# Kernel optimization log

Measured on AMD Instinct MI355X. Metric: run time of the kernel, lower is better.

## Reference

```python
import jax, jax.numpy as jnp
import numpy as np

B, T, D = 2, 2048, 1024
P, ALPHA, P_R = 512, 4, 64
HID = 16 * D
EPS = 1e-6


def rmsnorm(x, w):
    norm = jnp.sqrt(jnp.mean(x * x, axis=-1, keepdims=True) + EPS)
    return x * w / norm


def ssm_lowrank(t, F, b_r, c_r):
    # gated elementwise recurrence h_t = F_t * h_{t-1} + t_t, then low-rank correction
    Fs = jnp.moveaxis(F, 1, 0)   # (T,B,P)
    ts = jnp.moveaxis(t, 1, 0)   # (T,B,P)

    def step(h, inp):
        f, u = inp
        h = f * h + u
        return h, h

    h0 = jnp.zeros((t.shape[0], t.shape[2]), dtype=t.dtype)
    _, hs = jax.lax.scan(step, h0, (Fs, ts))
    h = jnp.moveaxis(hs, 0, 1)   # (B,T,P)
    t_tilde = t + jnp.einsum('btp,pr,rq->btq', h, b_r, c_r)
    return t_tilde


def setup_inputs() -> dict:
    key = jax.random.key(0)
    ks = jax.random.split(key, 11)
    s = lambda fan: 1.0 / np.sqrt(fan)
    return {
        'x':       jax.random.normal(ks[0], (B, T, D), jnp.float32),
        'w_norm1': jnp.ones((D,), jnp.float32),
        'w_toP':   jax.random.normal(ks[1], (D, P), jnp.float32) * s(D),
        'w_emb':   jax.random.normal(ks[2], (D, ALPHA * P), jnp.float32) * s(D),
        'w_f':     jax.random.normal(ks[3], (D, P), jnp.float32) * s(D),
        'b_r':     jax.random.normal(ks[4], (P, P_R), jnp.float32) * s(P),
        'c_r':     jax.random.normal(ks[5], (P_R, P), jnp.float32) * s(P_R),
        'w_fromP': jax.random.normal(ks[6], (P, D), jnp.float32) * s(P),
        'w_norm2': jnp.ones((D,), jnp.float32),
        'w_fc1':   jax.random.normal(ks[7], (D, HID), jnp.float32) * s(D),
        'w_fc2':   jax.random.normal(ks[8], (HID, D), jnp.float32) * s(HID),
    }


def reference(x, w_norm1, w_toP, w_emb, w_f, b_r, c_r, w_fromP, w_norm2, w_fc1, w_fc2):
    # ---- pre-LN CEPTA context path ----
    h1 = rmsnorm(x, w_norm1)
    pre_path = jnp.einsum('btd,dp->btp', h1, w_toP)                 # to_P
    U = jnp.einsum('btd,dk->btk', h1, w_emb).reshape(B, T, ALPHA, P)  # cepta_dense U
    Fgate = jax.nn.sigmoid(jnp.einsum('btd,dp->btp', h1, w_f))      # cepta_dense F
    Y = jax.nn.gelu(U)                                              # cepta_dense Y
    t = jnp.sum(Y, axis=2) + pre_path                               # router reduce='sum'
    t_tilde = ssm_lowrank(t, Fgate, b_r, c_r)                       # low-rank SSM
    y = jnp.einsum('btp,pd->btd', t_tilde, w_fromP)                 # from_P
    x = x + y
    # ---- pre-LN GELU MLP ----
    h2 = rmsnorm(x, w_norm2)
    z = jnp.einsum('bth,hd->btd', jax.nn.gelu(jnp.einsum('btd,dh->bth', h2, w_fc1)), w_fc2)
    return x + z
```

## Files before the change

### kernel.cpp

```cpp
#include <hip/hip_runtime.h>

typedef unsigned short u16;
typedef __bf16 bf16x8 __attribute__((ext_vector_type(8)));
typedef float f32x4 __attribute__((ext_vector_type(4)));
typedef int i32x4 __attribute__((ext_vector_type(4)));

__device__ inline u16 f2bf(float f) {
  union { float f; unsigned u; } v; v.f = f;
  unsigned u = v.u;
  unsigned r = (u + 0x7FFFu + ((u >> 16) & 1u)) >> 16;
  return (u16)r;
}
__device__ inline float bf2f(u16 u) {
  union { unsigned u; float f; } v; v.u = ((unsigned)u) << 16; return v.f;
}

__device__ inline float gelu_f(float x) {
  float t = 0.7978845608028654f * (x + 0.044715f * x * x * x);
  float a = __expf(-2.f * fabsf(t));
  float th = (1.f - a) / (1.f + a);
  th = copysignf(th, t);
  return 0.5f * x * (1.f + th);
}
__device__ inline float sigmoid_f(float x) { return 1.f / (1.f + __expf(-x)); }

__device__ __forceinline__ void gld16(const u16* g, u16* l) {
  __builtin_amdgcn_global_load_lds((const __attribute__((address_space(1))) void*)g,
                                   (__attribute__((address_space(3))) void*)l, 16, 0, 0);
}
__device__ __forceinline__ bf16x8 ld_frag(const u16* p) {
  return __builtin_bit_cast(bf16x8, *(const i32x4*)p);
}

__global__ void transpose_cvt(const float* __restrict__ in, u16* __restrict__ out,
                              int R, int C, int ldout) {
  __shared__ float tile[32][33];
  int c0 = blockIdx.x * 32, r0 = blockIdx.y * 32;
  int tx = threadIdx.x, ty = threadIdx.y;
#pragma unroll
  for (int i = 0; i < 32; i += 8) {
    int r = r0 + ty + i, c = c0 + tx;
    tile[ty + i][tx] = (r < R && c < C) ? in[(long)r * C + c] : 0.f;
  }
  __syncthreads();
#pragma unroll
  for (int i = 0; i < 32; i += 8) {
    int cc = c0 + ty + i, rr = r0 + tx;
    if (cc < C && rr < R) out[(long)cc * ldout + rr] = f2bf(tile[tx][ty + i]);
  }
}

__global__ __launch_bounds__(256) void rmsnorm_k(const float* __restrict__ x,
                                                 const float* __restrict__ w,
                                                 u16* __restrict__ out) {
  int row = blockIdx.x;
  int tid = threadIdx.x;
  const float4* xv = (const float4*)(x + (long)row * 1024);
  float4 v = xv[tid];
  float ss = v.x * v.x + v.y * v.y + v.z * v.z + v.w * v.w;
#pragma unroll
  for (int off = 32; off > 0; off >>= 1) ss += __shfl_down(ss, off);
  __shared__ float red[4];
  if ((tid & 63) == 0) red[tid >> 6] = ss;
  __syncthreads();
  float tot = red[0] + red[1] + red[2] + red[3];
  float scale = rsqrtf(tot * (1.f / 1024.f) + 1e-6f);
  const float4* wv4 = (const float4*)w;
  float4 wv = wv4[tid];
  ushort4 o;
  o.x = f2bf(v.x * wv.x * scale);
  o.y = f2bf(v.y * wv.y * scale);
  o.z = f2bf(v.z * wv.z * scale);
  o.w = f2bf(v.w * wv.w * scale);
  *((ushort4*)(out + (long)row * 1024) + tid) = o;
}

#define EPI_BF16 0
#define EPI_ROUTE1 1
#define EPI_ADD_BF16 2
#define EPI_ADD_F32 3
#define EPI_GELU_BF16 4
#define EPI_PART 5

#define VM4() asm volatile("s_waitcnt vmcnt(4)" ::: "memory")
#define VM0() asm volatile("s_waitcnt vmcnt(0)" ::: "memory")
#define BAR()                                   \
  asm volatile("" ::: "memory");                \
  __builtin_amdgcn_s_barrier();                 \
  asm volatile("" ::: "memory")

template <int EPI>
__global__ __launch_bounds__(512, 2) void gemm256(
    const u16* __restrict__ A, const u16* __restrict__ Bt,
    u16* __restrict__ obf, float* __restrict__ of32,
    int N, int K, int lda, int ldb) {
  __shared__ __align__(16) u16 sA[2][16384];
  __shared__ __align__(16) u16 sB[2][16384];
  const int tid = threadIdx.x;
  const int lane = tid & 63;
  const int wave = tid >> 6;
  const int wm = wave >> 2, wn = wave & 3;
  const int lane15 = lane & 15;

  const int gx = gridDim.x, gy = gridDim.y, gz = gridDim.z;
  const int nwg = gx * gy * gz;
  int orig = (blockIdx.z * gy + blockIdx.y) * gx + blockIdx.x;
  int id = ((nwg & 7) == 0) ? ((orig & 7) * (nwg >> 3) + (orig >> 3)) : orig;
  const int bx = id % gx;
  const int by = (id / gx) % gy;
  const int bz = id / (gx * gy);
  const int bm0 = by * 256, bn0 = bx * 256;
  const int kper = K / gz, koff = bz * kper;

  f32x4 acc[8][4];
  f32x4 zero = {0.f, 0.f, 0.f, 0.f};
#pragma unroll
  for (int m = 0; m < 8; ++m)
#pragma unroll
    for (int n = 0; n < 4; ++n) acc[m][n] = zero;

  const int grow = tid >> 2;
  const int gck = ((tid & 3) ^ ((tid >> 3) & 3)) << 3;
  const u16* pA0 = A + (long)(bm0 + grow) * lda + koff + gck;
  const u16* pB0 = Bt + (long)(bn0 + grow) * ldb + koff + gck;
  const u16* pA1 = pA0 + (long)128 * lda;
  const u16* pB1 = pB0 + (long)128 * ldb;
  const int wofs = wave << 9;

  const int coff = (((lane >> 4) ^ ((lane15 >> 1) & 3)) << 3);
  const u16* baseA = &sA[0][wm * 8192 + lane15 * 32 + coff];
  const u16* baseB = &sB[0][((wn >> 1) * 2) * 4096 + ((wn & 1) * 64 + lane15) * 32 + coff];

  const int nk = kper >> 6;
  const int nu = nk >> 1;

  gld16(pA0, &sA[0][0 * 4096 + wofs]);
  gld16(pA1, &sA[0][2 * 4096 + wofs]);
  gld16(pB0, &sB[0][0 * 4096 + wofs]);
  gld16(pB1, &sB[0][2 * 4096 + wofs]);
  gld16(pA0 + 32, &sA[0][1 * 4096 + wofs]);
  gld16(pA1 + 32, &sA[0][3 * 4096 + wofs]);
  gld16(pB0 + 32, &sB[0][1 * 4096 + wofs]);
  gld16(pB1 + 32, &sB[0][3 * 4096 + wofs]);

  bf16x8 av[4], bv[4];
#define DSRD_B256(P, kk)                                                     \
  _Pragma("unroll") for (int n = 0; n < 4; ++n)                              \
      bv[n] = ld_frag(baseB + (P)*16384 + (kk)*4096 + n * 512);
#define DSRD_A256(P, kk, mh)                                                 \
  _Pragma("unroll") for (int m = 0; m < 4; ++m)                              \
      av[m] = ld_frag(baseA + (P)*16384 + (kk)*4096 + (mh)*2048 + m * 512);
#define MFMA16(mh)                                                                   \
  __builtin_amdgcn_s_setprio(1);                                                     \
  _Pragma("unroll") for (int m = 0; m < 4; ++m)                                      \
      _Pragma("unroll") for (int n = 0; n < 4; ++n)                                  \
          acc[(mh)*4 + m][n] =                                                       \
              __builtin_amdgcn_mfma_f32_16x16x32_bf16(av[m], bv[n], acc[(mh)*4 + m][n], 0, 0, 0); \
  __builtin_amdgcn_s_setprio(0);

#define TILE256(P, STG, TOFS, LASTVM0)                       \
  VM4(); BAR();                                              \
  DSRD_B256(P, 0); DSRD_A256(P, 0, 0);                       \
  if (STG) { gld16(pA0 + (TOFS), &sA[(P) ^ 1][0 * 4096 + wofs]); gld16(pA1 + (TOFS), &sA[(P) ^ 1][2 * 4096 + wofs]); } \
  MFMA16(0);                                                 \
  DSRD_A256(P, 0, 1);                                        \
  if (STG) { gld16(pB0 + (TOFS), &sB[(P) ^ 1][0 * 4096 + wofs]); gld16(pB1 + (TOFS), &sB[(P) ^ 1][2 * 4096 + wofs]); } \
  MFMA16(1);                                                 \
  if (LASTVM0) { VM0(); } else { VM4(); }                    \
  BAR();                                                     \
  DSRD_B256(P, 1); DSRD_A256(P, 1, 0);                       \
  if (STG) { gld16(pA0 + (TOFS) + 32, &sA[(P) ^ 1][1 * 4096 + wofs]); gld16(pA1 + (TOFS) + 32, &sA[(P) ^ 1][3 * 4096 + wofs]); } \
  MFMA16(0);                                                 \
  DSRD_A256(P, 1, 1);                                        \
  if (STG) { gld16(pB0 + (TOFS) + 32, &sB[(P) ^ 1][1 * 4096 + wofs]); gld16(pB1 + (TOFS) + 32, &sB[(P) ^ 1][3 * 4096 + wofs]); } \
  MFMA16(1);

  for (int u = 0; u < nu; ++u) {
    const bool lp = (u == nu - 1);
    TILE256(0, true, 64, false);
    TILE256(1, !lp, 128, lp);
    pA0 += 128; pA1 += 128; pB0 += 128; pB1 += 128;
  }
#undef DSRD_B256
#undef DSRD_A256
#undef MFMA16
#undef TILE256

#pragma unroll
  for (int M = 0; M < 8; ++M) {
    int row_b = bm0 + wm * 128 + M * 16 + ((lane >> 4) << 2);
#pragma unroll
    for (int n = 0; n < 4; ++n) {
      int col = bn0 + wn * 64 + n * 16 + lane15;
#pragma unroll
      for (int j = 0; j < 4; ++j) {
        int row = row_b + j;
        float v = acc[M][n][j];
        if constexpr (EPI == EPI_GELU_BF16) {
          obf[(long)row * N + col] = f2bf(gelu_f(v));
        } else {
          of32[(long)bz * (4096L * 1024) + (long)row * N + col] = v;
        }
      }
    }
  }
}

template <int EPI>
__global__ __launch_bounds__(256, 2) void gemm128(
    const u16* __restrict__ A, const u16* __restrict__ Bt,
    u16* __restrict__ obf, float* __restrict__ of32, const float* __restrict__ add,
    u16* __restrict__ og, float* __restrict__ ofl,
    int N, int K, int lda, int ldb) {
  __shared__ __align__(16) u16 sA[2][8192];
  __shared__ __align__(16) u16 sB[2][8192];
  const int tid = threadIdx.x;
  const int lane = tid & 63;
  const int wave = tid >> 6;
  const int wm = wave >> 1, wn = wave & 1;
  const int lane15 = lane & 15;

  const int gx = gridDim.x, gy = gridDim.y;
  const int nwg = gx * gy;
  int orig = blockIdx.y * gx + blockIdx.x;
  int id = ((nwg & 7) == 0) ? ((orig & 7) * (nwg >> 3) + (orig >> 3)) : orig;
  const int bx = id % gx;
  const int by = id / gx;
  const int bm0 = by * 128, bn0 = bx * 128;

  f32x4 acc[4][4];
  f32x4 zero = {0.f, 0.f, 0.f, 0.f};
#pragma unroll
  for (int m = 0; m < 4; ++m)
#pragma unroll
    for (int n = 0; n < 4; ++n) acc[m][n] = zero;

  const int grow = tid >> 2;
  const int gck = ((tid & 3) ^ ((tid >> 3) & 3)) << 3;
  const u16* pA0 = A + (long)(bm0 + grow) * lda + gck;
  const u16* pB0 = Bt + (long)(bn0 + grow) * ldb + gck;
  const u16* pA1 = pA0 + (long)64 * lda;
  const u16* pB1 = pB0 + (long)64 * ldb;
  const int wofs = wave << 9;

  const int coff = (((lane >> 4) ^ ((lane15 >> 1) & 3)) << 3);
  const u16* baseA = &sA[0][wm * 2048 + lane15 * 32 + coff];
  const u16* baseB = &sB[0][wn * 2048 + lane15 * 32 + coff];

  const int nk = K >> 6;
  const int nu = nk >> 1;

  gld16(pA0, &sA[0][0 * 4096 + 0 * 2048 + wofs]);
  gld16(pA1, &sA[0][0 * 4096 + 1 * 2048 + wofs]);
  gld16(pB0, &sB[0][0 * 4096 + 0 * 2048 + wofs]);
  gld16(pB1, &sB[0][0 * 4096 + 1 * 2048 + wofs]);
  gld16(pA0 + 32, &sA[0][1 * 4096 + 0 * 2048 + wofs]);
  gld16(pA1 + 32, &sA[0][1 * 4096 + 1 * 2048 + wofs]);
  gld16(pB0 + 32, &sB[0][1 * 4096 + 0 * 2048 + wofs]);
  gld16(pB1 + 32, &sB[0][1 * 4096 + 1 * 2048 + wofs]);

  bf16x8 av[4], bv[4];
#define DSRD128(P, kk)                                                              \
  _Pragma("unroll") for (int m = 0; m < 4; ++m)                                     \
      av[m] = ld_frag(baseA + (P)*8192 + (kk)*4096 + m * 512);                      \
  _Pragma("unroll") for (int n = 0; n < 4; ++n)                                     \
      bv[n] = ld_frag(baseB + (P)*8192 + (kk)*4096 + n * 512);
#define MFMA16x()                                                                   \
  __builtin_amdgcn_s_setprio(1);                                                    \
  _Pragma("unroll") for (int m = 0; m < 4; ++m)                                     \
      _Pragma("unroll") for (int n = 0; n < 4; ++n)                                 \
          acc[m][n] = __builtin_amdgcn_mfma_f32_16x16x32_bf16(av[m], bv[n], acc[m][n], 0, 0, 0); \
  __builtin_amdgcn_s_setprio(0);
#define TILE128(P, STG, TOFS, LASTVM0)                                              \
  VM4(); BAR();                                                                     \
  DSRD128(P, 0);                                                                    \
  if (STG) {                                                                        \
    gld16(pA0 + (TOFS), &sA[(P) ^ 1][0 * 4096 + 0 * 2048 + wofs]);                  \
    gld16(pA1 + (TOFS), &sA[(P) ^ 1][0 * 4096 + 1 * 2048 + wofs]);                  \
    gld16(pB0 + (TOFS), &sB[(P) ^ 1][0 * 4096 + 0 * 2048 + wofs]);                  \
    gld16(pB1 + (TOFS), &sB[(P) ^ 1][0 * 4096 + 1 * 2048 + wofs]);                  \
  }                                                                                 \
  MFMA16x();                                                                        \
  if (LASTVM0) { VM0(); } else { VM4(); }                                           \
  BAR();                                                                            \
  DSRD128(P, 1);                                                                    \
  if (STG) {                                                                        \
    gld16(pA0 + (TOFS) + 32, &sA[(P) ^ 1][1 * 4096 + 0 * 2048 + wofs]);             \
    gld16(pA1 + (TOFS) + 32, &sA[(P) ^ 1][1 * 4096 + 1 * 2048 + wofs]);             \
    gld16(pB0 + (TOFS) + 32, &sB[(P) ^ 1][1 * 4096 + 0 * 2048 + wofs]);             \
    gld16(pB1 + (TOFS) + 32, &sB[(P) ^ 1][1 * 4096 + 1 * 2048 + wofs]);             \
  }                                                                                 \
  MFMA16x();

  for (int u = 0; u < nu; ++u) {
    const bool lp = (u == nu - 1);
    TILE128(0, true, 64, false);
    TILE128(1, !lp, 128, lp);
    pA0 += 128; pA1 += 128; pB0 += 128; pB1 += 128;
  }
#undef DSRD128
#undef MFMA16x
#undef TILE128

#pragma unroll
  for (int M = 0; M < 4; ++M) {
    int row_b = bm0 + wm * 64 + M * 16 + ((lane >> 4) << 2);
#pragma unroll
    for (int n = 0; n < 4; ++n) {
      int col = bn0 + wn * 64 + n * 16 + lane15;
#pragma unroll
      for (int j = 0; j < 4; ++j) {
        int row = row_b + j;
        float v = acc[M][n][j];
        if constexpr (EPI == EPI_BF16) {
          obf[(long)row * N + col] = f2bf(v);
        } else if constexpr (EPI == EPI_ADD_BF16) {
          long idx = (long)row * N + col;
          obf[idx] = f2bf(add[idx] + v);
        } else if constexpr (EPI == EPI_ADD_F32) {
          long idx = (long)row * N + col;
          of32[idx] = add[idx] + v;
        } else if constexpr (EPI == EPI_ROUTE1) {
          if (col < 512) of32[(long)row * 512 + col] = v;
          else if (col < 2560) og[(long)row * 2048 + (col - 512)] = f2bf(gelu_f(v));
          else ofl[(long)row * 512 + (col - 2560)] = sigmoid_f(v);
        }
      }
    }
  }
}

__global__ __launch_bounds__(256) void reduce4_k(const float* __restrict__ base,
                                                 const float* __restrict__ p,
                                                 float* __restrict__ o) {
  long i = (long)blockIdx.x * 256 + threadIdx.x;
  const long PL = 4096L * 1024 / 4;
  float4 b = ((const float4*)base)[i];
  float4 q0 = ((const float4*)p)[i];
  float4 q1 = ((const float4*)p)[i + PL];
  float4 q2 = ((const float4*)p)[i + 2 * PL];
  float4 q3 = ((const float4*)p)[i + 3 * PL];
  float4 r;
  r.x = b.x + q0.x + q1.x + q2.x + q3.x;
  r.y = b.y + q0.y + q1.y + q2.y + q3.y;
  r.z = b.z + q0.z + q1.z + q2.z + q3.z;
  r.w = b.w + q0.w + q1.w + q2.w + q3.w;
  ((float4*)o)[i] = r;
}

__global__ __launch_bounds__(256) void router_k(float* __restrict__ tb, const u16* __restrict__ G) {
  int i = blockIdx.x * 256 + threadIdx.x;
  int r = i >> 7, pq = i & 127;
  float4 t = ((float4*)tb)[i];
#pragma unroll
  for (int a = 0; a < 4; ++a) {
    ushort4 g = *((const ushort4*)(G + (long)r * 2048 + a * 512) + pq);
    t.x += bf2f(g.x); t.y += bf2f(g.y); t.z += bf2f(g.z); t.w += bf2f(g.w);
  }
  ((float4*)tb)[i] = t;
}

__global__ void scan_chunk(const float* __restrict__ tb, const float* __restrict__ F,
                           float* __restrict__ abuf, float* __restrict__ ubuf) {
  int b = blockIdx.x >> 5, c = blockIdx.x & 31, pidx = threadIdx.x;
  const float* fp = F + ((long)(b * 2048 + c * 64) * 512) + pidx;
  const float* up = tb + ((long)(b * 2048 + c * 64) * 512) + pidx;
  float A = 1.f, U = 0.f;
#pragma unroll 8
  for (int s = 0; s < 64; ++s) {
    float f = fp[(long)s * 512], u = up[(long)s * 512];
    A = f * A;
    U = f * U + u;
  }
  abuf[(b * 32 + c) * 512 + pidx] = A;
  ubuf[(b * 32 + c) * 512 + pidx] = U;
}

__global__ void scan_combine(const float* __restrict__ abuf, const float* __restrict__ ubuf,
                             float* __restrict__ hstart) {
  int b = blockIdx.x, pidx = threadIdx.x;
  float h = 0.f;
  for (int c = 0; c < 32; ++c) {
    hstart[(b * 32 + c) * 512 + pidx] = h;
    h = abuf[(b * 32 + c) * 512 + pidx] * h + ubuf[(b * 32 + c) * 512 + pidx];
  }
}

__global__ void scan_apply(const float* __restrict__ tb, const float* __restrict__ F,
                           const float* __restrict__ hstart, u16* __restrict__ hbf) {
  int b = blockIdx.x >> 5, c = blockIdx.x & 31, pidx = threadIdx.x;
  const float* fp = F + ((long)(b * 2048 + c * 64) * 512) + pidx;
  const float* up = tb + ((long)(b * 2048 + c * 64) * 512) + pidx;
  u16* op = hbf + ((long)(b * 2048 + c * 64) * 512) + pidx;
  float h = hstart[(b * 32 + c) * 512 + pidx];
#pragma unroll 8
  for (int s = 0; s < 64; ++s) {
    float f = fp[(long)s * 512], u = up[(long)s * 512];
    h = f * h + u;
    op[(long)s * 512] = f2bf(h);
  }
}

extern "C" void kernel_launch(void* const* d_in, const int* in_sizes, int n_in,
                              void* d_out, int out_size, void* d_ws, size_t ws_size,
                              hipStream_t stream) {
  const float* x       = (const float*)d_in[0];
  const float* w_norm1 = (const float*)d_in[1];
  const float* w_toP   = (const float*)d_in[2];
  const float* w_emb   = (const float*)d_in[3];
  const float* w_f     = (const float*)d_in[4];
  const float* b_r     = (const float*)d_in[5];
  const float* c_r     = (const float*)d_in[6];
  const float* w_fromP = (const float*)d_in[7];
  const float* w_norm2 = (const float*)d_in[8];
  const float* w_fc1   = (const float*)d_in[9];
  const float* w_fc2   = (const float*)d_in[10];
  float* out = (float*)d_out;

  char* base = (char*)d_ws;
  size_t off = 0;
  auto alloc = [&](size_t bytes) {
    void* r = base + off;
    off += (bytes + 255) & ~(size_t)255;
    return r;
  };
  u16* W1T     = (u16*)alloc((size_t)3072 * 1024 * 2);
  u16* WfromPT = (u16*)alloc((size_t)1024 * 512 * 2);
  u16* Wfc1T   = (u16*)alloc((size_t)16384 * 1024 * 2);
  u16* Wfc2T   = (u16*)alloc((size_t)1024 * 16384 * 2);
  u16* BrT     = (u16*)alloc((size_t)128 * 512 * 2);
  u16* CrT     = (u16*)alloc((size_t)512 * 128 * 2);
  u16* h1      = (u16*)alloc((size_t)4096 * 1024 * 2);
  float* G     = (float*)alloc((size_t)4096 * 2048 * 4);
  float* F     = (float*)alloc((size_t)4096 * 512 * 4);
  float* tb    = (float*)alloc((size_t)4096 * 512 * 4);
  float* abuf  = (float*)alloc((size_t)2 * 32 * 512 * 4);
  float* ubuf  = (float*)alloc((size_t)2 * 32 * 512 * 4);
  float* hstart= (float*)alloc((size_t)2 * 32 * 512 * 4);
  u16* hbf     = (u16*)alloc((size_t)4096 * 512 * 2);
  u16* g1buf   = (u16*)alloc((size_t)4096 * 128 * 2);
  u16* tt      = (u16*)alloc((size_t)4096 * 512 * 2);
  float* xmid  = (float*)alloc((size_t)4096 * 1024 * 4);
  u16* h2      = (u16*)alloc((size_t)4096 * 1024 * 2);
  u16* a3      = (u16*)alloc((size_t)4096 * 8192 * 2);
  float* part  = (float*)h1;
  u16* Gbf     = (u16*)G;
  (void)ws_size; (void)in_sizes; (void)n_in; (void)out_size;

  dim3 tpb(32, 8);
  transpose_cvt<<<dim3(16, 32), tpb, 0, stream>>>(w_toP, W1T, 1024, 512, 1024);
  transpose_cvt<<<dim3(64, 32), tpb, 0, stream>>>(w_emb, W1T + (size_t)512 * 1024, 1024, 2048, 1024);
  transpose_cvt<<<dim3(16, 32), tpb, 0, stream>>>(w_f, W1T + (size_t)2560 * 1024, 1024, 512, 1024);
  transpose_cvt<<<dim3(32, 16), tpb, 0, stream>>>(w_fromP, WfromPT, 512, 1024, 512);
  transpose_cvt<<<dim3(512, 32), tpb, 0, stream>>>(w_fc1, Wfc1T, 1024, 16384, 1024);
  transpose_cvt<<<dim3(32, 512), tpb, 0, stream>>>(w_fc2, Wfc2T, 16384, 1024, 16384);
  hipMemsetAsync(BrT, 0, (size_t)128 * 512 * 2, stream);
  hipMemsetAsync(CrT, 0, (size_t)512 * 128 * 2, stream);
  transpose_cvt<<<dim3(2, 16), tpb, 0, stream>>>(b_r, BrT, 512, 64, 512);
  transpose_cvt<<<dim3(16, 2), tpb, 0, stream>>>(c_r, CrT, 64, 512, 128);

  rmsnorm_k<<<4096, 256, 0, stream>>>(x, w_norm1, h1);

  gemm128<EPI_ROUTE1><<<dim3(24, 32), 256, 0, stream>>>(h1, W1T, nullptr, tb, nullptr, Gbf, F,
                                                        3072, 1024, 1024, 1024);
  router_k<<<2048, 256, 0, stream>>>(tb, Gbf);

  scan_chunk<<<64, 512, 0, stream>>>(tb, F, abuf, ubuf);
  scan_combine<<<2, 512, 0, stream>>>(abuf, ubuf, hstart);
  scan_apply<<<64, 512, 0, stream>>>(tb, F, hstart, hbf);

  gemm128<EPI_BF16><<<dim3(1, 32), 256, 0, stream>>>(hbf, BrT, g1buf, nullptr, nullptr, nullptr, nullptr,
                                                     128, 512, 512, 512);
  gemm128<EPI_ADD_BF16><<<dim3(4, 32), 256, 0, stream>>>(g1buf, CrT, tt, nullptr, tb, nullptr, nullptr,
                                                         512, 128, 128, 128);
  gemm128<EPI_ADD_F32><<<dim3(8, 32), 256, 0, stream>>>(tt, WfromPT, nullptr, xmid, x, nullptr, nullptr,
                                                        1024, 512, 512, 512);
  rmsnorm_k<<<4096, 256, 0, stream>>>(xmid, w_norm2, h2);

  for (int c = 0; c < 2; ++c) {
    gemm256<EPI_GELU_BF16><<<dim3(32, 16, 1), 512, 0, stream>>>(
        h2, Wfc1T + (size_t)c * 8192 * 1024, a3, nullptr,
        8192, 1024, 1024, 1024);
    gemm256<EPI_PART><<<dim3(4, 16, 4), 512, 0, stream>>>(
        a3, Wfc2T + (size_t)c * 8192, nullptr, part,
        1024, 8192, 8192, 16384);
    reduce4_k<<<4096, 256, 0, stream>>>((c == 0 ? xmid : out), part, out);
  }
}
```

Measured before the change: 547.2 us.

## Replace 256-tile MLP GEMMs with split-K 128-tile kernel and bf16 partials

Drops the 256x256 gemm256 kernel and runs both MLP GEMMs through gemm128, which gains split-K support via gridDim.z. fc2 now uses split-K of 2 instead of 4 and stores its partial sums as bf16 rather than fp32, and a new reduce kernel adds the two bf16 partials. The aim is to cut partial-sum traffic and the reduction cost. The tradeoff is less data reuse per tile in the large GEMMs and some loss of precision in the partials.

```diff
diff --git a/kernel.cpp b/kernel.cpp
--- a/kernel.cpp
+++ b/kernel.cpp
@@ -90,123 +90,6 @@
   asm volatile("" ::: "memory")
 
 template <int EPI>
-__global__ __launch_bounds__(512, 2) void gemm256(
-    const u16* __restrict__ A, const u16* __restrict__ Bt,
-    u16* __restrict__ obf, float* __restrict__ of32,
-    int N, int K, int lda, int ldb) {
-  __shared__ __align__(16) u16 sA[2][16384];
-  __shared__ __align__(16) u16 sB[2][16384];
-  const int tid = threadIdx.x;
-  const int lane = tid & 63;
-  const int wave = tid >> 6;
-  const int wm = wave >> 2, wn = wave & 3;
-  const int lane15 = lane & 15;
-
-  const int gx = gridDim.x, gy = gridDim.y, gz = gridDim.z;
-  const int nwg = gx * gy * gz;
-  int orig = (blockIdx.z * gy + blockIdx.y) * gx + blockIdx.x;
-  int id = ((nwg & 7) == 0) ? ((orig & 7) * (nwg >> 3) + (orig >> 3)) : orig;
-  const int bx = id % gx;
-  const int by = (id / gx) % gy;
-  const int bz = id / (gx * gy);
-  const int bm0 = by * 256, bn0 = bx * 256;
-  const int kper = K / gz, koff = bz * kper;
-
-  f32x4 acc[8][4];
-  f32x4 zero = {0.f, 0.f, 0.f, 0.f};
-#pragma unroll
-  for (int m = 0; m < 8; ++m)
-#pragma unroll
-    for (int n = 0; n < 4; ++n) acc[m][n] = zero;
-
-  const int grow = tid >> 2;
-  const int gck = ((tid & 3) ^ ((tid >> 3) & 3)) << 3;
-  const u16* pA0 = A + (long)(bm0 + grow) * lda + koff + gck;
-  const u16* pB0 = Bt + (long)(bn0 + grow) * ldb + koff + gck;
-  const u16* pA1 = pA0 + (long)128 * lda;
-  const u16* pB1 = pB0 + (long)128 * ldb;
-  const int wofs = wave << 9;
-
-  const int coff = (((lane >> 4) ^ ((lane15 >> 1) & 3)) << 3);
-  const u16* baseA = &sA[0][wm * 8192 + lane15 * 32 + coff];
-  const u16* baseB = &sB[0][((wn >> 1) * 2) * 4096 + ((wn & 1) * 64 + lane15) * 32 + coff];
-
-  const int nk = kper >> 6;
-  const int nu = nk >> 1;
-
-  gld16(pA0, &sA[0][0 * 4096 + wofs]);
-  gld16(pA1, &sA[0][2 * 4096 + wofs]);
-  gld16(pB0, &sB[0][0 * 4096 + wofs]);
-  gld16(pB1, &sB[0][2 * 4096 + wofs]);
-  gld16(pA0 + 32, &sA[0][1 * 4096 + wofs]);
-  gld16(pA1 + 32, &sA[0][3 * 4096 + wofs]);
-  gld16(pB0 + 32, &sB[0][1 * 4096 + wofs]);
-  gld16(pB1 + 32, &sB[0][3 * 4096 + wofs]);
-
-  bf16x8 av[4], bv[4];
-#define DSRD_B256(P, kk)                                                     \
-  _Pragma("unroll") for (int n = 0; n < 4; ++n)                              \
-      bv[n] = ld_frag(baseB + (P)*16384 + (kk)*4096 + n * 512);
-#define DSRD_A256(P, kk, mh)                                                 \
-  _Pragma("unroll") for (int m = 0; m < 4; ++m)                              \
-      av[m] = ld_frag(baseA + (P)*16384 + (kk)*4096 + (mh)*2048 + m * 512);
-#define MFMA16(mh)                                                                   \
-  __builtin_amdgcn_s_setprio(1);                                                     \
-  _Pragma("unroll") for (int m = 0; m < 4; ++m)                                      \
-      _Pragma("unroll") for (int n = 0; n < 4; ++n)                                  \
-          acc[(mh)*4 + m][n] =                                                       \
-              __builtin_amdgcn_mfma_f32_16x16x32_bf16(av[m], bv[n], acc[(mh)*4 + m][n], 0, 0, 0); \
-  __builtin_amdgcn_s_setprio(0);
-
-#define TILE256(P, STG, TOFS, LASTVM0)                       \
-  VM4(); BAR();                                              \
-  DSRD_B256(P, 0); DSRD_A256(P, 0, 0);                       \
-  if (STG) { gld16(pA0 + (TOFS), &sA[(P) ^ 1][0 * 4096 + wofs]); gld16(pA1 + (TOFS), &sA[(P) ^ 1][2 * 4096 + wofs]); } \
-  MFMA16(0);                                                 \
-  DSRD_A256(P, 0, 1);                                        \
-  if (STG) { gld16(pB0 + (TOFS), &sB[(P) ^ 1][0 * 4096 + wofs]); gld16(pB1 + (TOFS), &sB[(P) ^ 1][2 * 4096 + wofs]); } \
-  MFMA16(1);                                                 \
-  if (LASTVM0) { VM0(); } else { VM4(); }                    \
-  BAR();                                                     \
-  DSRD_B256(P, 1); DSRD_A256(P, 1, 0);                       \
-  if (STG) { gld16(pA0 + (TOFS) + 32, &sA[(P) ^ 1][1 * 4096 + wofs]); gld16(pA1 + (TOFS) + 32, &sA[(P) ^ 1][3 * 4096 + wofs]); } \
-  MFMA16(0);                                                 \
-  DSRD_A256(P, 1, 1);                                        \
-  if (STG) { gld16(pB0 + (TOFS) + 32, &sB[(P) ^ 1][1 * 4096 + wofs]); gld16(pB1 + (TOFS) + 32, &sB[(P) ^ 1][3 * 4096 + wofs]); } \
-  MFMA16(1);
-
-  for (int u = 0; u < nu; ++u) {
-    const bool lp = (u == nu - 1);
-    TILE256(0, true, 64, false);
-    TILE256(1, !lp, 128, lp);
-    pA0 += 128; pA1 += 128; pB0 += 128; pB1 += 128;
-  }
-#undef DSRD_B256
-#undef DSRD_A256
-#undef MFMA16
-#undef TILE256
-
-#pragma unroll
-  for (int M = 0; M < 8; ++M) {
-    int row_b = bm0 + wm * 128 + M * 16 + ((lane >> 4) << 2);
-#pragma unroll
-    for (int n = 0; n < 4; ++n) {
-      int col = bn0 + wn * 64 + n * 16 + lane15;
-#pragma unroll
-      for (int j = 0; j < 4; ++j) {
-        int row = row_b + j;
-        float v = acc[M][n][j];
-        if constexpr (EPI == EPI_GELU_BF16) {
-          obf[(long)row * N + col] = f2bf(gelu_f(v));
-        } else {
-          of32[(long)bz * (4096L * 1024) + (long)row * N + col] = v;
-        }
-      }
-    }
-  }
-}
-
-template <int EPI>
 __global__ __launch_bounds__(256, 2) void gemm128(
     const u16* __restrict__ A, const u16* __restrict__ Bt,
     u16* __restrict__ obf, float* __restrict__ of32, const float* __restrict__ add,
@@ -220,13 +103,15 @@
   const int wm = wave >> 1, wn = wave & 1;
   const int lane15 = lane & 15;
 
-  const int gx = gridDim.x, gy = gridDim.y;
-  const int nwg = gx * gy;
-  int orig = blockIdx.y * gx + blockIdx.x;
+  const int gx = gridDim.x, gy = gridDim.y, gz = gridDim.z;
+  const int nwg = gx * gy * gz;
+  int orig = (blockIdx.z * gy + blockIdx.y) * gx + blockIdx.x;
   int id = ((nwg & 7) == 0) ? ((orig & 7) * (nwg >> 3) + (orig >> 3)) : orig;
   const int bx = id % gx;
-  const int by = id / gx;
+  const int by = (id / gx) % gy;
+  const int bz = id / (gx * gy);
   const int bm0 = by * 128, bn0 = bx * 128;
+  const int kper = K / gz, koff = bz * kper;
 
   f32x4 acc[4][4];
   f32x4 zero = {0.f, 0.f, 0.f, 0.f};
@@ -237,8 +122,8 @@
 
   const int grow = tid >> 2;
   const int gck = ((tid & 3) ^ ((tid >> 3) & 3)) << 3;
-  const u16* pA0 = A + (long)(bm0 + grow) * lda + gck;
-  const u16* pB0 = Bt + (long)(bn0 + grow) * ldb + gck;
+  const u16* pA0 = A + (long)(bm0 + grow) * lda + koff + gck;
+  const u16* pB0 = Bt + (long)(bn0 + grow) * ldb + koff + gck;
   const u16* pA1 = pA0 + (long)64 * lda;
   const u16* pB1 = pB0 + (long)64 * ldb;
   const int wofs = wave << 9;
@@ -247,7 +132,7 @@
   const u16* baseA = &sA[0][wm * 2048 + lane15 * 32 + coff];
   const u16* baseB = &sB[0][wn * 2048 + lane15 * 32 + coff];
 
-  const int nk = K >> 6;
+  const int nk = kper >> 6;
   const int nu = nk >> 1;
 
   gld16(pA0, &sA[0][0 * 4096 + 0 * 2048 + wofs]);
@@ -320,7 +205,11 @@
         } else if constexpr (EPI == EPI_ADD_F32) {
           long idx = (long)row * N + col;
           of32[idx] = add[idx] + v;
-        } else if constexpr (EPI == EPI_ROUTE1) {
+        } else if constexpr (EPI == EPI_GELU_BF16) {
+          obf[(long)row * N + col] = f2bf(gelu_f(v));
+        } else if constexpr (EPI == EPI_PART) {
+          obf[(long)bz * (4096L * 1024) + (long)row * N + col] = f2bf(v);
+        } else {
           if (col < 512) of32[(long)row * 512 + col] = v;
           else if (col < 2560) og[(long)row * 2048 + (col - 512)] = f2bf(gelu_f(v));
           else ofl[(long)row * 512 + (col - 2560)] = sigmoid_f(v);
@@ -330,21 +219,19 @@
   }
 }
 
-__global__ __launch_bounds__(256) void reduce4_k(const float* __restrict__ base,
-                                                 const float* __restrict__ p,
-                                                 float* __restrict__ o) {
+__global__ __launch_bounds__(256) void reduce2b_k(const float* __restrict__ base,
+                                                  const u16* __restrict__ p,
+                                                  float* __restrict__ o) {
   long i = (long)blockIdx.x * 256 + threadIdx.x;
-  const long PL = 4096L * 1024 / 4;
+  const long PL = 4096L * 1024;
   float4 b = ((const float4*)base)[i];
-  float4 q0 = ((const float4*)p)[i];
-  float4 q1 = ((const float4*)p)[i + PL];
-  float4 q2 = ((const float4*)p)[i + 2 * PL];
-  float4 q3 = ((const float4*)p)[i + 3 * PL];
+  ushort4 q0 = ((const ushort4*)p)[i];
+  ushort4 q1 = *((const ushort4*)(p + PL) + i);
   float4 r;
-  r.x = b.x + q0.x + q1.x + q2.x + q3.x;
-  r.y = b.y + q0.y + q1.y + q2.y + q3.y;
-  r.z = b.z + q0.z + q1.z + q2.z + q3.z;
-  r.w = b.w + q0.w + q1.w + q2.w + q3.w;
+  r.x = b.x + bf2f(q0.x) + bf2f(q1.x);
+  r.y = b.y + bf2f(q0.y) + bf2f(q1.y);
+  r.z = b.z + bf2f(q0.z) + bf2f(q1.z);
+  r.w = b.w + bf2f(q0.w) + bf2f(q1.w);
   ((float4*)o)[i] = r;
 }
 
@@ -443,7 +330,7 @@
   float* xmid  = (float*)alloc((size_t)4096 * 1024 * 4);
   u16* h2      = (u16*)alloc((size_t)4096 * 1024 * 2);
   u16* a3      = (u16*)alloc((size_t)4096 * 8192 * 2);
-  float* part  = (float*)h1;
+  u16* partb   = (u16*)h1;
   u16* Gbf     = (u16*)G;
   (void)ws_size; (void)in_sizes; (void)n_in; (void)out_size;
 
@@ -478,12 +365,12 @@
   rmsnorm_k<<<4096, 256, 0, stream>>>(xmid, w_norm2, h2);
 
   for (int c = 0; c < 2; ++c) {
-    gemm256<EPI_GELU_BF16><<<dim3(32, 16, 1), 512, 0, stream>>>(
-        h2, Wfc1T + (size_t)c * 8192 * 1024, a3, nullptr,
+    gemm128<EPI_GELU_BF16><<<dim3(64, 32), 256, 0, stream>>>(
+        h2, Wfc1T + (size_t)c * 8192 * 1024, a3, nullptr, nullptr, nullptr, nullptr,
         8192, 1024, 1024, 1024);
-    gemm256<EPI_PART><<<dim3(4, 16, 4), 512, 0, stream>>>(
-        a3, Wfc2T + (size_t)c * 8192, nullptr, part,
+    gemm128<EPI_PART><<<dim3(8, 32, 2), 256, 0, stream>>>(
+        a3, Wfc2T + (size_t)c * 8192, partb, nullptr, nullptr, nullptr, nullptr,
         1024, 8192, 8192, 16384);
-    reduce4_k<<<4096, 256, 0, stream>>>((c == 0 ? xmid : out), part, out);
-  }
-}
+    reduce2b_k<<<4096, 256, 0, stream>>>((c == 0 ? xmid : out), partb, out);
+  }
+}
```

After: 581.5 us. +6.3%, slower.

## Restructure 256x256 GEMM into a 4-stage 32-wide K pipeline

Applied to the files above, without the earlier changes.

Replaces the double-buffered 64-wide K tiles with four 32-wide K stages in LDS, keeping three stages of global loads in flight ahead of compute. The LDS layout and fragment addressing change, and the epilogue row mapping is adjusted to match. The goal is to hide global memory latency better, at the cost of one barrier per 32-K step instead of per 32-K half-tile and a different LDS layout that could bring bank conflicts or correctness risk.

```diff
diff --git a/kernel.cpp b/kernel.cpp
--- a/kernel.cpp
+++ b/kernel.cpp
@@ -82,6 +82,7 @@
 #define EPI_GELU_BF16 4
 #define EPI_PART 5
 
+#define VM8() asm volatile("s_waitcnt vmcnt(8)" ::: "memory")
 #define VM4() asm volatile("s_waitcnt vmcnt(4)" ::: "memory")
 #define VM0() asm volatile("s_waitcnt vmcnt(0)" ::: "memory")
 #define BAR()                                   \
@@ -94,8 +95,8 @@
     const u16* __restrict__ A, const u16* __restrict__ Bt,
     u16* __restrict__ obf, float* __restrict__ of32,
     int N, int K, int lda, int ldb) {
-  __shared__ __align__(16) u16 sA[2][16384];
-  __shared__ __align__(16) u16 sB[2][16384];
+  __shared__ __align__(16) u16 sA[4][8192];
+  __shared__ __align__(16) u16 sB[4][8192];
   const int tid = threadIdx.x;
   const int lane = tid & 63;
   const int wave = tid >> 6;
@@ -128,28 +129,29 @@
   const int wofs = wave << 9;
 
   const int coff = (((lane >> 4) ^ ((lane15 >> 1) & 3)) << 3);
-  const u16* baseA = &sA[0][wm * 8192 + lane15 * 32 + coff];
-  const u16* baseB = &sB[0][((wn >> 1) * 2) * 4096 + ((wn & 1) * 64 + lane15) * 32 + coff];
-
-  const int nk = kper >> 6;
-  const int nu = nk >> 1;
-
-  gld16(pA0, &sA[0][0 * 4096 + wofs]);
-  gld16(pA1, &sA[0][2 * 4096 + wofs]);
-  gld16(pB0, &sB[0][0 * 4096 + wofs]);
-  gld16(pB1, &sB[0][2 * 4096 + wofs]);
-  gld16(pA0 + 32, &sA[0][1 * 4096 + wofs]);
-  gld16(pA1 + 32, &sA[0][3 * 4096 + wofs]);
-  gld16(pB0 + 32, &sB[0][1 * 4096 + wofs]);
-  gld16(pB1 + 32, &sB[0][3 * 4096 + wofs]);
+  const u16* baseA = &sA[0][wm * 4096 + lane15 * 32 + coff];
+  const u16* baseB = &sB[0][wn * 2048 + lane15 * 32 + coff];
+
+  const int nkh = kper >> 5;
+  const int U = nkh >> 2;
+
+#define STAGE256(S, T)                          \
+  gld16(pA0 + (T), &sA[S][0 * 4096 + wofs]);    \
+  gld16(pA1 + (T), &sA[S][1 * 4096 + wofs]);    \
+  gld16(pB0 + (T), &sB[S][0 * 4096 + wofs]);    \
+  gld16(pB1 + (T), &sB[S][1 * 4096 + wofs]);
+
+  STAGE256(0, 0)
+  STAGE256(1, 32)
+  STAGE256(2, 64)
 
   bf16x8 av[4], bv[4];
-#define DSRD_B256(P, kk)                                                     \
+#define DSRD_B256(S)                                                         \
   _Pragma("unroll") for (int n = 0; n < 4; ++n)                              \
-      bv[n] = ld_frag(baseB + (P)*16384 + (kk)*4096 + n * 512);
-#define DSRD_A256(P, kk, mh)                                                 \
+      bv[n] = ld_frag(baseB + (S)*8192 + n * 512);
+#define DSRD_A256(S, mh)                                                     \
   _Pragma("unroll") for (int m = 0; m < 4; ++m)                              \
-      av[m] = ld_frag(baseA + (P)*16384 + (kk)*4096 + (mh)*2048 + m * 512);
+      av[m] = ld_frag(baseA + (S)*8192 + (mh)*2048 + m * 512);
 #define MFMA16(mh)                                                                   \
   __builtin_amdgcn_s_setprio(1);                                                     \
   _Pragma("unroll") for (int m = 0; m < 4; ++m)                                      \
@@ -158,37 +160,34 @@
               __builtin_amdgcn_mfma_f32_16x16x32_bf16(av[m], bv[n], acc[(mh)*4 + m][n], 0, 0, 0); \
   __builtin_amdgcn_s_setprio(0);
 
-#define TILE256(P, STG, TOFS, LASTVM0)                       \
-  VM4(); BAR();                                              \
-  DSRD_B256(P, 0); DSRD_A256(P, 0, 0);                       \
-  if (STG) { gld16(pA0 + (TOFS), &sA[(P) ^ 1][0 * 4096 + wofs]); gld16(pA1 + (TOFS), &sA[(P) ^ 1][2 * 4096 + wofs]); } \
-  MFMA16(0);                                                 \
-  DSRD_A256(P, 0, 1);                                        \
-  if (STG) { gld16(pB0 + (TOFS), &sB[(P) ^ 1][0 * 4096 + wofs]); gld16(pB1 + (TOFS), &sB[(P) ^ 1][2 * 4096 + wofs]); } \
-  MFMA16(1);                                                 \
-  if (LASTVM0) { VM0(); } else { VM4(); }                    \
-  BAR();                                                     \
-  DSRD_B256(P, 1); DSRD_A256(P, 1, 0);                       \
-  if (STG) { gld16(pA0 + (TOFS) + 32, &sA[(P) ^ 1][1 * 4096 + wofs]); gld16(pA1 + (TOFS) + 32, &sA[(P) ^ 1][3 * 4096 + wofs]); } \
-  MFMA16(0);                                                 \
-  DSRD_A256(P, 1, 1);                                        \
-  if (STG) { gld16(pB0 + (TOFS) + 32, &sB[(P) ^ 1][1 * 4096 + wofs]); gld16(pB1 + (TOFS) + 32, &sB[(P) ^ 1][3 * 4096 + wofs]); } \
+#define KH256(S, VMW, STG, T)                   \
+  VMW(); BAR();                                 \
+  DSRD_B256(S); DSRD_A256(S, 0);                \
+  if (STG) { STAGE256((S + 3) & 3, T) }         \
+  MFMA16(0);                                    \
+  DSRD_A256(S, 1);                              \
   MFMA16(1);
 
-  for (int u = 0; u < nu; ++u) {
-    const bool lp = (u == nu - 1);
-    TILE256(0, true, 64, false);
-    TILE256(1, !lp, 128, lp);
+  for (int u = 0; u < U - 1; ++u) {
+    KH256(0, VM8, 1, 96)
+    KH256(1, VM8, 1, 128)
+    KH256(2, VM8, 1, 160)
+    KH256(3, VM8, 1, 192)
     pA0 += 128; pA1 += 128; pB0 += 128; pB1 += 128;
   }
+  KH256(0, VM8, 1, 96)
+  KH256(1, VM8, 0, 0)
+  KH256(2, VM4, 0, 0)
+  KH256(3, VM0, 0, 0)
+#undef STAGE256
 #undef DSRD_B256
 #undef DSRD_A256
 #undef MFMA16
-#undef TILE256
+#undef KH256
 
 #pragma unroll
   for (int M = 0; M < 8; ++M) {
-    int row_b = bm0 + wm * 128 + M * 16 + ((lane >> 4) << 2);
+    int row_b = bm0 + wm * 128 + (M >> 2) * 64 + (M & 3) * 16 + ((lane >> 4) << 2);
 #pragma unroll
     for (int n = 0; n < 4; ++n) {
       int col = bn0 + wn * 64 + n * 16 + lane15;
```

Measured after the change: 555.3 us. About the same (+1.5%).

## Store FC2 split-K partials in bf16 and merge reductions into one pass

Applied to the files above, without the earlier changes.

The FC2 split-K GEMM now writes its partial sums as bf16 instead of fp32. The split factor per chunk drops from 4 to 2, and both hidden-dimension chunks write into distinct slices of one partial buffer. A single bf16-reading reduce kernel then sums the four slices onto the residual, replacing two fp32 reduce launches. This cuts partial-sum write and read traffic and removes one kernel launch. In exchange it loses precision in the partials and halves the grid of each FC2 launch, which may lower GPU utilisation.

```diff
diff --git a/kernel.cpp b/kernel.cpp
--- a/kernel.cpp
+++ b/kernel.cpp
@@ -199,7 +199,7 @@
         if constexpr (EPI == EPI_GELU_BF16) {
           obf[(long)row * N + col] = f2bf(gelu_f(v));
         } else {
-          of32[(long)bz * (4096L * 1024) + (long)row * N + col] = v;
+          obf[(long)bz * (4096L * 1024) + (long)row * N + col] = f2bf(v);
         }
       }
     }
@@ -330,21 +330,21 @@
   }
 }
 
-__global__ __launch_bounds__(256) void reduce4_k(const float* __restrict__ base,
-                                                 const float* __restrict__ p,
-                                                 float* __restrict__ o) {
+__global__ __launch_bounds__(256) void reduce4b_k(const float* __restrict__ base,
+                                                  const u16* __restrict__ p,
+                                                  float* __restrict__ o) {
   long i = (long)blockIdx.x * 256 + threadIdx.x;
-  const long PL = 4096L * 1024 / 4;
+  const long PL = 4096L * 1024;
   float4 b = ((const float4*)base)[i];
-  float4 q0 = ((const float4*)p)[i];
-  float4 q1 = ((const float4*)p)[i + PL];
-  float4 q2 = ((const float4*)p)[i + 2 * PL];
-  float4 q3 = ((const float4*)p)[i + 3 * PL];
+  ushort4 q0 = *((const ushort4*)(p) + i);
+  ushort4 q1 = *((const ushort4*)(p + PL) + i);
+  ushort4 q2 = *((const ushort4*)(p + 2 * PL) + i);
+  ushort4 q3 = *((const ushort4*)(p + 3 * PL) + i);
   float4 r;
-  r.x = b.x + q0.x + q1.x + q2.x + q3.x;
-  r.y = b.y + q0.y + q1.y + q2.y + q3.y;
-  r.z = b.z + q0.z + q1.z + q2.z + q3.z;
-  r.w = b.w + q0.w + q1.w + q2.w + q3.w;
+  r.x = b.x + bf2f(q0.x) + bf2f(q1.x) + bf2f(q2.x) + bf2f(q3.x);
+  r.y = b.y + bf2f(q0.y) + bf2f(q1.y) + bf2f(q2.y) + bf2f(q3.y);
+  r.z = b.z + bf2f(q0.z) + bf2f(q1.z) + bf2f(q2.z) + bf2f(q3.z);
+  r.w = b.w + bf2f(q0.w) + bf2f(q1.w) + bf2f(q2.w) + bf2f(q3.w);
   ((float4*)o)[i] = r;
 }
 
@@ -443,7 +443,7 @@
   float* xmid  = (float*)alloc((size_t)4096 * 1024 * 4);
   u16* h2      = (u16*)alloc((size_t)4096 * 1024 * 2);
   u16* a3      = (u16*)alloc((size_t)4096 * 8192 * 2);
-  float* part  = (float*)h1;
+  u16* partb   = (u16*)h1;
   u16* Gbf     = (u16*)G;
   (void)ws_size; (void)in_sizes; (void)n_in; (void)out_size;
 
@@ -481,9 +481,9 @@
     gemm256<EPI_GELU_BF16><<<dim3(32, 16, 1), 512, 0, stream>>>(
         h2, Wfc1T + (size_t)c * 8192 * 1024, a3, nullptr,
         8192, 1024, 1024, 1024);
-    gemm256<EPI_PART><<<dim3(4, 16, 4), 512, 0, stream>>>(
-        a3, Wfc2T + (size_t)c * 8192, nullptr, part,
+    gemm256<EPI_PART><<<dim3(4, 16, 2), 512, 0, stream>>>(
+        a3, Wfc2T + (size_t)c * 8192, partb + (size_t)c * 2 * 4096 * 1024, nullptr,
         1024, 8192, 8192, 16384);
-    reduce4_k<<<4096, 256, 0, stream>>>((c == 0 ? xmid : out), part, out);
-  }
-}
+  }
+  reduce4b_k<<<4096, 256, 0, stream>>>(xmid, partb, out);
+}
```

After: 588.0 us. +7.4%, slower.
